# Kernel tuning notes

Measured on AMD Instinct MI355X. Metric: run time of the kernel, lower is better.

Reference implementation:

```python
import jax, jax.numpy as jnp
import numpy as np

M = 262144      # total tokens
K = 64          # n_channels (input dim)
N = 64          # expert_size (output dim)
E = 8           # n_experts


def setup_inputs() -> dict:
    key = jax.random.key(0)
    k1, k2, k3 = jax.random.split(key, 3)
    x = jax.random.normal(k1, (M, K), dtype=jnp.float32)
    sel = jax.random.randint(k2, (M,), 0, E, dtype=jnp.int32)
    w = jax.random.normal(k3, (E, K, N), dtype=jnp.float32)
    return {"x": x, "sel": sel, "w": w}


def reference(x, sel, w):
    # cvmm: out[m] = x[m] @ w[sel[m]]  (per-token expert GEMM)
    # Loop over the small fixed expert set; accumulate masked dense GEMMs
    # instead of materializing w[sel] ([M,K,N], which would be huge).
    E_ = w.shape[0]
    out = jnp.zeros((x.shape[0], w.shape[2]), dtype=x.dtype)
    for e in range(E_):
        mask = (sel == e)[:, None]           # [M,1]
        out = out + jnp.where(mask, x @ w[e], jnp.zeros((), x.dtype))
    return out
```

## Files before the change

kernel.cpp:

```cpp
#include <hip/hip_runtime.h>


typedef __bf16 bf16x8 __attribute__((ext_vector_type(8)));
typedef __bf16 bf16x4 __attribute__((ext_vector_type(4)));
typedef float  floatx4 __attribute__((ext_vector_type(4)));

__global__ __launch_bounds__(256) void wpack_kernel(
    const float* __restrict__ w, bf16x8* __restrict__ wp)
{
    const int id   = blockIdx.x * 256 + threadIdx.x;
    const int lane = id & 63;
    const int nt   = (id >> 6) & 3;
    const int t    = (id >> 8) & 1;
    const int e    = id >> 9;
    const int q = lane >> 4, l16 = lane & 15;
    const float* src = w + (((e * 64) + t * 32 + q * 8) * 64) + nt * 16 + l16;
    bf16x8 f;
#pragma unroll
    for (int j = 0; j < 8; ++j) f[j] = (__bf16)src[j * 64];
    wp[id] = f;
}

__global__ __launch_bounds__(256, 8) void cvmm_kernel(
    const float* __restrict__ x,
    const int* __restrict__ sel,
    const bf16x8* __restrict__ wp,
    float* __restrict__ out)
{
    __shared__ __align__(16) unsigned char xls[128 * 128];
    __shared__ unsigned int sortLds[128];
    __shared__ int wcLds[16];

    const int T    = threadIdx.x;
    const int lane = T & 63;
    const int wv   = T >> 6;
    const int q    = lane >> 4;
    const int l16  = lane & 15;
    const int n0   = wv << 4;

    const long tok0 = (long)blockIdx.x * 128;

    const float* xb = x + tok0 * 64;
    floatx4 R[8];
#pragma unroll
    for (int i = 0; i < 8; ++i)
        R[i] = *(const floatx4*)(xb + i * 1024 + 4 * T);

    int s = 0, myrank = 0;
    if (T < 128) {
        s = sel[tok0 + T];
        const unsigned long long lt = (1ull << lane) - 1;
#pragma unroll
        for (int e = 0; e < 8; ++e) {
            unsigned long long m = __ballot(s == e);
            if (s == e) myrank = __popcll(m & lt);
            if (lane == 0) wcLds[wv * 8 + e] = __popcll(m);
        }
    }
    __syncthreads();
    if (T < 128) {
        int bb = 0;
#pragma unroll
        for (int e2 = 0; e2 < 8; ++e2) {
            const int tot = wcLds[e2] + wcLds[8 + e2];
            if (e2 < s) bb += tot;
        }
        const int wb = (wv == 1) ? wcLds[s] : 0;
        sortLds[bb + wb + myrank] = (unsigned)T | ((unsigned)s << 8);
    }

    const int wrow = T >> 4;
    const int g    = (T & 15) >> 1;
    const int half = (T & 1) * 8;
#pragma unroll
    for (int i = 0; i < 8; ++i) {
        const int row = i * 16 + wrow;
        bf16x4 v;
        v[0] = (__bf16)R[i][0]; v[1] = (__bf16)R[i][1];
        v[2] = (__bf16)R[i][2]; v[3] = (__bf16)R[i][3];
        *(bf16x4*)(xls + row * 128 + (((g) ^ (row & 7)) << 4) + half) = v;
    }
    __syncthreads();

    bf16x8 zf;
#pragma unroll
    for (int j = 0; j < 8; ++j) zf[j] = (__bf16)0.0f;

    const bf16x8* wpw = wp + wv * 64 + lane;

#pragma unroll
    for (int i = 0; i < 8; ++i) {
        const unsigned u = sortLds[i * 16 + l16];
        const int tokL = (int)(u & 255u);
        const int el   = (int)(u >> 8);
        const bf16x8 af0 = *(const bf16x8*)(xls + tokL * 128 + (((q)     ^ (tokL & 7)) << 4));
        const bf16x8 af1 = *(const bf16x8*)(xls + tokL * 128 + (((q + 4) ^ (tokL & 7)) << 4));
        const int elo = __builtin_amdgcn_readfirstlane(el);
        const int ehi = __builtin_amdgcn_readlane(el, 15);

        floatx4 acc = {0.0f, 0.0f, 0.0f, 0.0f};
        if (elo == ehi) {
            const bf16x8 wf0 = wpw[elo * 512];
            const bf16x8 wf1 = wpw[elo * 512 + 256];
            acc = __builtin_amdgcn_mfma_f32_16x16x32_bf16(wf0, af0, acc, 0, 0, 0);
            acc = __builtin_amdgcn_mfma_f32_16x16x32_bf16(wf1, af1, acc, 0, 0, 0);
        } else {
            for (int e = elo; e <= ehi; ++e) {
                const bf16x8 wf0 = wpw[e * 512];
                const bf16x8 wf1 = wpw[e * 512 + 256];
                const bool ok = (el == e);
                const bf16x8 am0 = ok ? af0 : zf;
                const bf16x8 am1 = ok ? af1 : zf;
                acc = __builtin_amdgcn_mfma_f32_16x16x32_bf16(wf0, am0, acc, 0, 0, 0);
                acc = __builtin_amdgcn_mfma_f32_16x16x32_bf16(wf1, am1, acc, 0, 0, 0);
            }
        }
        float* op = out + (tok0 + tokL) * 64 + n0 + (q << 2);
        *(floatx4*)op = acc;
    }
}

extern "C" void kernel_launch(void* const* d_in, const int* in_sizes, int n_in,
                              void* d_out, int out_size, void* d_ws, size_t ws_size,
                              hipStream_t stream) {
    const float* x   = (const float*)d_in[0];
    const int*   sel = (const int*)d_in[1];
    const float* w   = (const float*)d_in[2];
    float*       out = (float*)d_out;

    const int M = in_sizes[0] / 64;
    bf16x8* wp = (bf16x8*)d_ws;

    wpack_kernel<<<16, 256, 0, stream>>>(w, wp);
    cvmm_kernel<<<M / 128, 256, 0, stream>>>(x, sel, wp, out);
}
```

Baseline: 129.2 us.

## Process four token chunks per block with double-buffered register prefetch of x

Each block now handles 512 tokens in four 128-token chunks. Register sets RA and RB hold x for alternating chunks, so the load of chunk c+2 is issued before chunk c is computed and global latency can overlap MFMA work. The counting sort now runs in a single wave and builds an inverse slot map, so x rows are written to LDS already in sorted order and the A-fragment reads become sequential. The cost is more registers per thread (occupancy hint lowered from 8 to 2), fewer blocks in the grid, and extra barriers per chunk.

```diff
diff --git a/kernel.cpp b/kernel.cpp
--- a/kernel.cpp
+++ b/kernel.cpp
@@ -4,6 +4,10 @@
 typedef __bf16 bf16x8 __attribute__((ext_vector_type(8)));
 typedef __bf16 bf16x4 __attribute__((ext_vector_type(4)));
 typedef float  floatx4 __attribute__((ext_vector_type(4)));
+
+#define NCHUNK 4
+#define CT 128
+#define BLK_TOK (NCHUNK * CT)
 
 __global__ __launch_bounds__(256) void wpack_kernel(
     const float* __restrict__ w, bf16x8* __restrict__ wp)
@@ -21,15 +25,22 @@
     wp[id] = f;
 }
 
-__global__ __launch_bounds__(256, 8) void cvmm_kernel(
+#define BAR() do {                                         \
+    __builtin_amdgcn_sched_barrier(0);                     \
+    asm volatile("s_waitcnt lgkmcnt(0)" ::: "memory");     \
+    __builtin_amdgcn_s_barrier();                          \
+    __builtin_amdgcn_sched_barrier(0);                     \
+} while (0)
+
+__global__ __launch_bounds__(256, 2) void cvmm_kernel(
     const float* __restrict__ x,
     const int* __restrict__ sel,
     const bf16x8* __restrict__ wp,
     float* __restrict__ out)
 {
-    __shared__ __align__(16) unsigned char xls[128 * 128];
-    __shared__ unsigned int sortLds[128];
-    __shared__ int wcLds[16];
+    __shared__ __align__(16) unsigned char xls[2][16384];
+    __shared__ unsigned int sortLds[2][128];
+    __shared__ unsigned int invLds[2][128];
 
     const int T    = threadIdx.x;
     const int lane = T & 63;
@@ -38,49 +49,13 @@
     const int l16  = lane & 15;
     const int n0   = wv << 4;
 
-    const long tok0 = (long)blockIdx.x * 128;
+    const int wrow = T >> 4;
+    const int gl   = (T & 15) >> 1;
+    const int half = (T & 1) * 8;
+    const int roffA = ((q)     ^ (l16 & 7)) << 4;
+    const int roffB = ((q + 4) ^ (l16 & 7)) << 4;
 
-    const float* xb = x + tok0 * 64;
-    floatx4 R[8];
-#pragma unroll
-    for (int i = 0; i < 8; ++i)
-        R[i] = *(const floatx4*)(xb + i * 1024 + 4 * T);
-
-    int s = 0, myrank = 0;
-    if (T < 128) {
-        s = sel[tok0 + T];
-        const unsigned long long lt = (1ull << lane) - 1;
-#pragma unroll
-        for (int e = 0; e < 8; ++e) {
-            unsigned long long m = __ballot(s == e);
-            if (s == e) myrank = __popcll(m & lt);
-            if (lane == 0) wcLds[wv * 8 + e] = __popcll(m);
-        }
-    }
-    __syncthreads();
-    if (T < 128) {
-        int bb = 0;
-#pragma unroll
-        for (int e2 = 0; e2 < 8; ++e2) {
-            const int tot = wcLds[e2] + wcLds[8 + e2];
-            if (e2 < s) bb += tot;
-        }
-        const int wb = (wv == 1) ? wcLds[s] : 0;
-        sortLds[bb + wb + myrank] = (unsigned)T | ((unsigned)s << 8);
-    }
-
-    const int wrow = T >> 4;
-    const int g    = (T & 15) >> 1;
-    const int half = (T & 1) * 8;
-#pragma unroll
-    for (int i = 0; i < 8; ++i) {
-        const int row = i * 16 + wrow;
-        bf16x4 v;
-        v[0] = (__bf16)R[i][0]; v[1] = (__bf16)R[i][1];
-        v[2] = (__bf16)R[i][2]; v[3] = (__bf16)R[i][3];
-        *(bf16x4*)(xls + row * 128 + (((g) ^ (row & 7)) << 4) + half) = v;
-    }
-    __syncthreads();
+    const long base = (long)blockIdx.x * BLK_TOK;
 
     bf16x8 zf;
 #pragma unroll
@@ -88,36 +63,109 @@
 
     const bf16x8* wpw = wp + wv * 64 + lane;
 
+    int sA0 = 0, sA1 = 0, sB0 = 0, sB1 = 0;
+    if (wv == 0) {
+        const int* sp = sel + base;
+        sA0 = sp[lane];      sA1 = sp[64 + lane];
+        sB0 = sp[CT + lane]; sB1 = sp[CT + 64 + lane];
+    }
+    floatx4 RA[8], RB[8];
+    {
+        const float* xc = x + base * 64;
 #pragma unroll
-    for (int i = 0; i < 8; ++i) {
-        const unsigned u = sortLds[i * 16 + l16];
-        const int tokL = (int)(u & 255u);
-        const int el   = (int)(u >> 8);
-        const bf16x8 af0 = *(const bf16x8*)(xls + tokL * 128 + (((q)     ^ (tokL & 7)) << 4));
-        const bf16x8 af1 = *(const bf16x8*)(xls + tokL * 128 + (((q + 4) ^ (tokL & 7)) << 4));
-        const int elo = __builtin_amdgcn_readfirstlane(el);
-        const int ehi = __builtin_amdgcn_readlane(el, 15);
+        for (int i = 0; i < 8; ++i)
+            RA[i] = *(const floatx4*)(xc + i * 1024 + 4 * T);
+#pragma unroll
+        for (int i = 0; i < 8; ++i)
+            RB[i] = *(const floatx4*)(xc + CT * 64 + i * 1024 + 4 * T);
+    }
 
-        floatx4 acc = {0.0f, 0.0f, 0.0f, 0.0f};
-        if (elo == ehi) {
-            const bf16x8 wf0 = wpw[elo * 512];
-            const bf16x8 wf1 = wpw[elo * 512 + 256];
-            acc = __builtin_amdgcn_mfma_f32_16x16x32_bf16(wf0, af0, acc, 0, 0, 0);
-            acc = __builtin_amdgcn_mfma_f32_16x16x32_bf16(wf1, af1, acc, 0, 0, 0);
-        } else {
-            for (int e = elo; e <= ehi; ++e) {
-                const bf16x8 wf0 = wpw[e * 512];
-                const bf16x8 wf1 = wpw[e * 512 + 256];
-                const bool ok = (el == e);
-                const bf16x8 am0 = ok ? af0 : zf;
-                const bf16x8 am1 = ok ? af1 : zf;
-                acc = __builtin_amdgcn_mfma_f32_16x16x32_bf16(wf0, am0, acc, 0, 0, 0);
-                acc = __builtin_amdgcn_mfma_f32_16x16x32_bf16(wf1, am1, acc, 0, 0, 0);
-            }
-        }
-        float* op = out + (tok0 + tokL) * 64 + n0 + (q << 2);
-        *(floatx4*)op = acc;
+#define CHUNK_BODY(c, RX, sX0, sX1)                                          \
+    {                                                                        \
+        const int buf = (c) & 1;                                             \
+                          \
+        if (wv == 0) {                                                       \
+            const unsigned long long lt = (1ull << lane) - 1;                \
+            int slot0 = 0, slot1 = 0, pref = 0;                              \
+            _Pragma("unroll")                                                \
+            for (int e = 0; e < 8; ++e) {                                    \
+                unsigned long long m0 = __ballot(sX0 == e);                  \
+                unsigned long long m1 = __ballot(sX1 == e);                  \
+                if (sX0 == e) slot0 = pref + __popcll(m0 & lt);              \
+                if (sX1 == e) slot1 = pref + __popcll(m0) + __popcll(m1 & lt);\
+                pref += __popcll(m0) + __popcll(m1);                         \
+            }                                                                \
+            invLds[buf][lane]      = (unsigned)slot0;                        \
+            invLds[buf][64 + lane] = (unsigned)slot1;                        \
+            sortLds[buf][slot0] = (unsigned)lane        | ((unsigned)sX0 << 8); \
+            sortLds[buf][slot1] = (unsigned)(64 + lane) | ((unsigned)sX1 << 8); \
+        }                                                                    \
+        BAR();                                                               \
+              \
+        {                                                                    \
+            unsigned char* lb = xls[buf];                                    \
+            _Pragma("unroll")                                                \
+            for (int i = 0; i < 8; ++i) {                                    \
+                const int slot = (int)invLds[buf][i * 16 + wrow];            \
+                bf16x4 v;                                                    \
+                v[0] = (__bf16)RX[i][0]; v[1] = (__bf16)RX[i][1];            \
+                v[2] = (__bf16)RX[i][2]; v[3] = (__bf16)RX[i][3];            \
+                *(bf16x4*)(lb + slot * 128 + ((gl ^ (slot & 7)) << 4) + half) = v; \
+            }                                                                \
+        }                                                                    \
+         \
+        if (wv == 0 && (c) + 2 < NCHUNK) {                                   \
+            const int* sp = sel + base + ((c) + 2) * CT;                     \
+            sX0 = sp[lane]; sX1 = sp[64 + lane];                             \
+        }                                                                    \
+        BAR();                                                               \
+                      \
+        if ((c) + 2 < NCHUNK) {                                              \
+            const float* xc = x + (base + ((c) + 2) * CT) * 64;              \
+            _Pragma("unroll")                                                \
+            for (int i = 0; i < 8; ++i)                                      \
+                RX[i] = *(const floatx4*)(xc + i * 1024 + 4 * T);            \
+        }                                                                    \
+                        \
+        {                                                                    \
+            const unsigned char* lb = xls[buf];                              \
+            const long ct0 = base + (c) * CT;                                \
+            _Pragma("unroll")                                                \
+            for (int i = 0; i < 8; ++i) {                                    \
+                const unsigned u = sortLds[buf][i * 16 + l16];               \
+                const int tokL = (int)(u & 255u);                            \
+                const int el   = (int)(u >> 8);                              \
+                const int rb2  = (i * 16 + l16) * 128;                       \
+                const bf16x8 af0 = *(const bf16x8*)(lb + rb2 + roffA);       \
+                const bf16x8 af1 = *(const bf16x8*)(lb + rb2 + roffB);       \
+                const int elo = __builtin_amdgcn_readfirstlane(el);          \
+                const int ehi = __builtin_amdgcn_readlane(el, 15);           \
+                floatx4 acc = {0.0f, 0.0f, 0.0f, 0.0f};                      \
+                if (elo == ehi) {                                            \
+                    acc = __builtin_amdgcn_mfma_f32_16x16x32_bf16(           \
+                              wpw[elo * 512],       af0, acc, 0, 0, 0);      \
+                    acc = __builtin_amdgcn_mfma_f32_16x16x32_bf16(           \
+                              wpw[elo * 512 + 256], af1, acc, 0, 0, 0);      \
+                } else {                                                     \
+                    for (int e = elo; e <= ehi; ++e) {                       \
+                        const bool ok = (el == e);                           \
+                        acc = __builtin_amdgcn_mfma_f32_16x16x32_bf16(       \
+                                  wpw[e * 512],       ok ? af0 : zf, acc, 0, 0, 0); \
+                        acc = __builtin_amdgcn_mfma_f32_16x16x32_bf16(       \
+                                  wpw[e * 512 + 256], ok ? af1 : zf, acc, 0, 0, 0); \
+                    }                                                        \
+                }                                                            \
+                float* op = out + (ct0 + tokL) * 64 + n0 + (q << 2);         \
+                *(floatx4*)op = acc;                                         \
+            }                                                                \
+        }                                                                    \
     }
+
+    CHUNK_BODY(0, RA, sA0, sA1)
+    CHUNK_BODY(1, RB, sB0, sB1)
+    CHUNK_BODY(2, RA, sA0, sA1)
+    CHUNK_BODY(3, RB, sB0, sB1)
+#undef CHUNK_BODY
 }
 
 extern "C" void kernel_launch(void* const* d_in, const int* in_sizes, int n_in,
@@ -132,5 +180,5 @@
     bf16x8* wp = (bf16x8*)d_ws;
 
     wpack_kernel<<<16, 256, 0, stream>>>(w, wp);
-    cvmm_kernel<<<M / 128, 256, 0, stream>>>(x, sel, wp, out);
+    cvmm_kernel<<<M / BLK_TOK, 256, 0, stream>>>(x, sel, wp, out);
 }
```

Measured after the change: 125.8 us. 2.6% less time.

## Preload all expert weights, scatter x to sorted slots, stage output through LDS

Applied to the files above, without the earlier changes.

Each wave now preloads all eight experts' packed bf16 weight fragments into registers up front, so the MFMA loop no longer issues dependent global loads per expert. The sort moves to a single wave that also builds an inverse map. The bf16 x tile is then written to LDS directly in sorted order, which removes the indirect token lookup at MFMA operand load. Results go into a padded LDS buffer and are written back as fully coalesced contiguous rows instead of scattered 16-byte stores. In exchange the kernel uses many more registers and LDS, and launch bounds drop occupancy from 8 to 3 blocks.

```diff
diff --git a/kernel.cpp b/kernel.cpp
--- a/kernel.cpp
+++ b/kernel.cpp
@@ -4,6 +4,8 @@
 typedef __bf16 bf16x8 __attribute__((ext_vector_type(8)));
 typedef __bf16 bf16x4 __attribute__((ext_vector_type(4)));
 typedef float  floatx4 __attribute__((ext_vector_type(4)));
+
+#define CT 128
 
 __global__ __launch_bounds__(256) void wpack_kernel(
     const float* __restrict__ w, bf16x8* __restrict__ wp)
@@ -21,24 +23,30 @@
     wp[id] = f;
 }
 
-__global__ __launch_bounds__(256, 8) void cvmm_kernel(
+__global__ __launch_bounds__(256, 3) void cvmm_kernel(
     const float* __restrict__ x,
     const int* __restrict__ sel,
     const bf16x8* __restrict__ wp,
     float* __restrict__ out)
 {
-    __shared__ __align__(16) unsigned char xls[128 * 128];
-    __shared__ unsigned int sortLds[128];
-    __shared__ int wcLds[16];
+    __shared__ __align__(16) unsigned char xls[CT * 128];
+    __shared__ __align__(16) unsigned char obuf[CT * 272];
+    __shared__ unsigned int sortLds[CT];
+    __shared__ unsigned int invLds[CT];
 
     const int T    = threadIdx.x;
     const int lane = T & 63;
     const int wv   = T >> 6;
     const int q    = lane >> 4;
     const int l16  = lane & 15;
-    const int n0   = wv << 4;
 
-    const long tok0 = (long)blockIdx.x * 128;
+    const long tok0 = (long)blockIdx.x * CT;
+
+    int s0 = 0, s1 = 0;
+    if (wv == 0) {
+        s0 = sel[tok0 + lane];
+        s1 = sel[tok0 + 64 + lane];
+    }
 
     const float* xb = x + tok0 * 64;
     floatx4 R[8];
@@ -46,77 +54,96 @@
     for (int i = 0; i < 8; ++i)
         R[i] = *(const floatx4*)(xb + i * 1024 + 4 * T);
 
-    int s = 0, myrank = 0;
-    if (T < 128) {
-        s = sel[tok0 + T];
+    const bf16x8* wpw = wp + wv * 64 + lane;
+    floatx4 bfp[8][2];
+#pragma unroll
+    for (int e = 0; e < 8; ++e) {
+#pragma unroll
+        for (int t = 0; t < 2; ++t)
+            bfp[e][t] = __builtin_bit_cast(floatx4, wpw[e * 512 + t * 256]);
+    }
+#pragma unroll
+    for (int e = 0; e < 8; ++e) {
+        asm volatile("" : "+v"(bfp[e][0]), "+v"(bfp[e][1]));
+    }
+
+    if (wv == 0) {
         const unsigned long long lt = (1ull << lane) - 1;
+        int slot0 = 0, slot1 = 0, pref = 0;
 #pragma unroll
         for (int e = 0; e < 8; ++e) {
-            unsigned long long m = __ballot(s == e);
-            if (s == e) myrank = __popcll(m & lt);
-            if (lane == 0) wcLds[wv * 8 + e] = __popcll(m);
+            unsigned long long m0 = __ballot(s0 == e);
+            unsigned long long m1 = __ballot(s1 == e);
+            if (s0 == e) slot0 = pref + __popcll(m0 & lt);
+            if (s1 == e) slot1 = pref + __popcll(m0) + __popcll(m1 & lt);
+            pref += __popcll(m0) + __popcll(m1);
+        }
+        invLds[lane]      = (unsigned)slot0;
+        invLds[64 + lane] = (unsigned)slot1;
+        sortLds[slot0] = (unsigned)lane        | ((unsigned)s0 << 8);
+        sortLds[slot1] = (unsigned)(64 + lane) | ((unsigned)s1 << 8);
+    }
+    __syncthreads();
+
+    {
+        const int wrow = T >> 4;
+        const int gl   = (T & 15) >> 1;
+        const int half = (T & 1) * 8;
+#pragma unroll
+        for (int i = 0; i < 8; ++i) {
+            const int slot = (int)invLds[i * 16 + wrow];
+            bf16x4 v;
+            v[0] = (__bf16)R[i][0]; v[1] = (__bf16)R[i][1];
+            v[2] = (__bf16)R[i][2]; v[3] = (__bf16)R[i][3];
+            *(bf16x4*)(xls + slot * 128 + ((gl ^ (slot & 7)) << 4) + half) = v;
         }
     }
     __syncthreads();
-    if (T < 128) {
-        int bb = 0;
+
+    {
+        const int roffA = ((q)     ^ (l16 & 7)) << 4;
+        const int roffB = ((q + 4) ^ (l16 & 7)) << 4;
+        bf16x8 zf;
 #pragma unroll
-        for (int e2 = 0; e2 < 8; ++e2) {
-            const int tot = wcLds[e2] + wcLds[8 + e2];
-            if (e2 < s) bb += tot;
+        for (int j = 0; j < 8; ++j) zf[j] = (__bf16)0.0f;
+
+#pragma unroll
+        for (int i = 0; i < 8; ++i) {
+            const unsigned u = sortLds[i * 16 + l16];
+            const int tokL = (int)(u & 255u);
+            const int el   = (int)(u >> 8);
+            const int rb   = (i * 16 + l16) * 128;
+            const bf16x8 af0 = *(const bf16x8*)(xls + rb + roffA);
+            const bf16x8 af1 = *(const bf16x8*)(xls + rb + roffB);
+            const int elo = __builtin_amdgcn_readfirstlane(el);
+            const int ehi = __builtin_amdgcn_readlane(el, 15);
+
+            floatx4 acc = {0.0f, 0.0f, 0.0f, 0.0f};
+#pragma unroll
+            for (int e = 0; e < 8; ++e) {
+                if (e >= elo && e <= ehi) {
+                    const bool ok = (el == e);
+                    acc = __builtin_amdgcn_mfma_f32_16x16x32_bf16(
+                              __builtin_bit_cast(bf16x8, bfp[e][0]),
+                              ok ? af0 : zf, acc, 0, 0, 0);
+                    acc = __builtin_amdgcn_mfma_f32_16x16x32_bf16(
+                              __builtin_bit_cast(bf16x8, bfp[e][1]),
+                              ok ? af1 : zf, acc, 0, 0, 0);
+                }
+            }
+            *(floatx4*)(obuf + tokL * 272 + (wv * 4 + q) * 16) = acc;
         }
-        const int wb = (wv == 1) ? wcLds[s] : 0;
-        sortLds[bb + wb + myrank] = (unsigned)T | ((unsigned)s << 8);
-    }
-
-    const int wrow = T >> 4;
-    const int g    = (T & 15) >> 1;
-    const int half = (T & 1) * 8;
-#pragma unroll
-    for (int i = 0; i < 8; ++i) {
-        const int row = i * 16 + wrow;
-        bf16x4 v;
-        v[0] = (__bf16)R[i][0]; v[1] = (__bf16)R[i][1];
-        v[2] = (__bf16)R[i][2]; v[3] = (__bf16)R[i][3];
-        *(bf16x4*)(xls + row * 128 + (((g) ^ (row & 7)) << 4) + half) = v;
     }
     __syncthreads();
 
-    bf16x8 zf;
+    {
+        float* og = out + tok0 * 64;
 #pragma unroll
-    for (int j = 0; j < 8; ++j) zf[j] = (__bf16)0.0f;
-
-    const bf16x8* wpw = wp + wv * 64 + lane;
-
-#pragma unroll
-    for (int i = 0; i < 8; ++i) {
-        const unsigned u = sortLds[i * 16 + l16];
-        const int tokL = (int)(u & 255u);
-        const int el   = (int)(u >> 8);
-        const bf16x8 af0 = *(const bf16x8*)(xls + tokL * 128 + (((q)     ^ (tokL & 7)) << 4));
-        const bf16x8 af1 = *(const bf16x8*)(xls + tokL * 128 + (((q + 4) ^ (tokL & 7)) << 4));
-        const int elo = __builtin_amdgcn_readfirstlane(el);
-        const int ehi = __builtin_amdgcn_readlane(el, 15);
-
-        floatx4 acc = {0.0f, 0.0f, 0.0f, 0.0f};
-        if (elo == ehi) {
-            const bf16x8 wf0 = wpw[elo * 512];
-            const bf16x8 wf1 = wpw[elo * 512 + 256];
-            acc = __builtin_amdgcn_mfma_f32_16x16x32_bf16(wf0, af0, acc, 0, 0, 0);
-            acc = __builtin_amdgcn_mfma_f32_16x16x32_bf16(wf1, af1, acc, 0, 0, 0);
-        } else {
-            for (int e = elo; e <= ehi; ++e) {
-                const bf16x8 wf0 = wpw[e * 512];
-                const bf16x8 wf1 = wpw[e * 512 + 256];
-                const bool ok = (el == e);
-                const bf16x8 am0 = ok ? af0 : zf;
-                const bf16x8 am1 = ok ? af1 : zf;
-                acc = __builtin_amdgcn_mfma_f32_16x16x32_bf16(wf0, am0, acc, 0, 0, 0);
-                acc = __builtin_amdgcn_mfma_f32_16x16x32_bf16(wf1, am1, acc, 0, 0, 0);
-            }
+        for (int i = 0; i < 8; ++i) {
+            const int G = i * 256 + T;
+            const floatx4 v = *(const floatx4*)(obuf + (G >> 4) * 272 + (G & 15) * 16);
+            *(floatx4*)(og + G * 4) = v;
         }
-        float* op = out + (tok0 + tokL) * 64 + n0 + (q << 2);
-        *(floatx4*)op = acc;
     }
 }
 
@@ -132,5 +159,5 @@
     bf16x8* wp = (bf16x8*)d_ws;
 
     wpack_kernel<<<16, 256, 0, stream>>>(w, wp);
-    cvmm_kernel<<<M / 128, 256, 0, stream>>>(x, sel, wp, out);
+    cvmm_kernel<<<M / CT, 256, 0, stream>>>(x, sel, wp, out);
 }
```

After: 121.4 us. -6.0%, faster.
